# Optimization experiments

Hardware: AMD Instinct MI355X
Metric: run time of the kernel (lower is better)

The kernel has to match this reference:

```python
import jax, jax.numpy as jnp
import numpy as np

B, S, E = 4, 2048, 2048
NH, NKV, HD = 16, 4, 128  # num_heads, num_kv_heads, head_dim
GROUP = NH // NKV


def setup_inputs() -> dict:
    key = jax.random.key(0)
    ks = jax.random.split(key, 6)
    sc = 0.02
    return {
        "hidden_states": jax.random.normal(ks[0], (B, S, E), dtype=jnp.float32),
        "q_w": jax.random.normal(ks[1], (E, NH * HD), dtype=jnp.float32) * sc,
        "k_w": jax.random.normal(ks[2], (E, NKV * HD), dtype=jnp.float32) * sc,
        "v_w": jax.random.normal(ks[3], (E, NKV * HD), dtype=jnp.float32) * sc,
        "out_w": jax.random.normal(ks[4], (NH * HD, E), dtype=jnp.float32) * sc,
        "out_b": jnp.zeros((E,), dtype=jnp.float32),
    }


def reference(hidden_states, q_w, k_w, v_w, out_w, out_b):
    x = hidden_states
    # projections (no bias on q/k/v, bias on out_proj)
    q = (x @ q_w).reshape(B, S, NH, HD).transpose(0, 2, 1, 3)    # [B,NH,S,HD]
    k = (x @ k_w).reshape(B, S, NKV, HD).transpose(0, 2, 1, 3)   # [B,NKV,S,HD]
    v = (x @ v_w).reshape(B, S, NKV, HD).transpose(0, 2, 1, 3)   # [B,NKV,S,HD]

    # GQA: each kv head serves GROUP consecutive query heads (matches loop order)
    k_exp = jnp.repeat(k, GROUP, axis=1)  # [B,NH,S,HD]
    v_exp = jnp.repeat(v, GROUP, axis=1)

    # GPT-Neo: fp32 attention, NO 1/sqrt(d) scaling
    qf = q.astype(jnp.float32)
    kf = k_exp.astype(jnp.float32)
    scores = jnp.einsum("bhqd,bhkd->bhqk", qf, kf)  # [B,NH,S,S]

    causal = jnp.tril(jnp.ones((S, S), dtype=bool))[None, None]
    mask_value = jnp.finfo(scores.dtype).min
    scores = jnp.where(causal, scores, mask_value)

    attn = jax.nn.softmax(scores, axis=-1).astype(v.dtype)
    ctx = jnp.einsum("bhqk,bhkd->bhqd", attn, v_exp)  # [B,NH,S,HD]

    out = ctx.transpose(0, 2, 1, 3).reshape(B, S, NH * HD)
    return out @ out_w + out_b
```

## Files before the change

### kernel.cpp

```cpp
#include <hip/hip_runtime.h>

typedef unsigned short u16;
typedef unsigned int   u32;
typedef __attribute__((ext_vector_type(8))) _Float16 f16x8;
typedef __attribute__((ext_vector_type(2))) __fp16   fp16x2;
typedef __attribute__((ext_vector_type(4))) float    f32x4;

#define LOG2E 1.44269504088896340f

__device__ __forceinline__ u16 f2h(float x) {
  union { _Float16 h; u16 u; } c;
  c.h = (_Float16)x;
  return c.u;
}
__device__ __forceinline__ u32 pk2(float a, float b) {
  union { fp16x2 h; u32 u; } c;
  c.h = __builtin_amdgcn_cvt_pkrtz(a, b);
  return c.u;
}
__device__ __forceinline__ void swap32(u32& a, u32& b) {
  asm volatile("v_permlane32_swap_b32 %0, %1" : "+v"(a), "+v"(b));
}
__device__ __forceinline__ void swap16(u32& a, u32& b) {
  asm volatile("v_permlane16_swap_b32 %0, %1" : "+v"(a), "+v"(b));
}
__device__ __forceinline__ void gload16(const u16* g, u16* l) {
  __builtin_amdgcn_global_load_lds(
      (const __attribute__((address_space(1))) void*)g,
      (__attribute__((address_space(3))) void*)l, 16, 0, 0);
}
__device__ __forceinline__ f32x4 MFMA(f16x8 a, f16x8 b, f32x4 c) {
  return __builtin_amdgcn_mfma_f32_16x16x32_f16(a, b, c, 0, 0, 0);
}

__global__ void conv_f16(const float4* __restrict__ src, u16* __restrict__ d, int n4) {
  int i = blockIdx.x * 256 + threadIdx.x;
  if (i >= n4) return;
  float4 v = src[i];
  union { u16 u[4]; uint2 q; } H;
  H.u[0] = f2h(v.x); H.u[1] = f2h(v.y); H.u[2] = f2h(v.z); H.u[3] = f2h(v.w);
  *(uint2*)&d[(size_t)i * 4] = H.q;
}

__global__ void transpose_f16(const float* __restrict__ src, int K, int N,
                              u16* __restrict__ d, int rowOff) {
  __shared__ float t[32][33];
  int n0 = blockIdx.x * 32, k0 = blockIdx.y * 32;
  int tx = threadIdx.x, ty = threadIdx.y;
#pragma unroll
  for (int i = 0; i < 4; ++i)
    t[ty + 8 * i][tx] = src[(size_t)(k0 + ty + 8 * i) * N + n0 + tx];
  __syncthreads();
#pragma unroll
  for (int i = 0; i < 4; ++i) {
    int n = n0 + ty + 8 * i, k = k0 + tx;
    d[(size_t)(rowOff + n) * 2048 + k] = f2h(t[tx][ty + 8 * i]);
  }
}

__global__ __launch_bounds__(512) void gemm_qkv(
    const u16* __restrict__ A, const u16* __restrict__ B,
    u16* __restrict__ Qf, u16* __restrict__ Kf, u16* __restrict__ VT) {
  const int K = 2048;
  const int NS = K / 32;
  __shared__ u16 As[3][256 * 32];
  __shared__ u16 Bs[3][128 * 32];
  int tid = threadIdx.x;
  int l = tid & 63, w = tid >> 6;
  int lr = l & 15, lg = l >> 4;
  int wr = w >> 1, wc = w & 1;
  int r0 = tid >> 2;
  int ssrc = (((tid & 3) ^ ((r0 >> 1) & 3))) * 8;
  size_t half = (size_t)128 * K;
  int swz = (lr >> 1) & 3;
  int aoff = (wr * 64 + lr) * 32 + (lg ^ swz) * 8;
  int boff = (wc * 64 + lr) * 32 + (lg ^ swz) * 8;

  for (int job = blockIdx.x; job < 768; job += 512) {
    int lidx = (job & 7) * 96 + (job >> 3);
    int bx = lidx % 24, by = lidx / 24;
    int rowA = by * 256, colB = bx * 128;
    const u16* ga = A + (size_t)(rowA + r0) * K + ssrc;
    const u16* gb = B + (size_t)(colB + r0) * K + ssrc;
    f32x4 acc[4][4] = {};

    gload16(ga, &As[0][tid * 8]);
    gload16(ga + half, &As[0][4096 + tid * 8]);
    gload16(gb, &Bs[0][tid * 8]);
    gload16(ga + 32, &As[1][tid * 8]);
    gload16(ga + 32 + half, &As[1][4096 + tid * 8]);
    gload16(gb + 32, &Bs[1][tid * 8]);
    asm volatile("s_waitcnt vmcnt(3)" ::: "memory");
    __builtin_amdgcn_sched_barrier(0);
    __builtin_amdgcn_s_barrier();
    __builtin_amdgcn_sched_barrier(0);

    for (int t = 0; t < NS; ++t) {
      int cur = t % 3, nxt = (t + 2) % 3;
      bool pre = (t + 2 < NS);
      int kb2 = (t + 2) * 32;
      f16x8 ah[4], bh[4];
#pragma unroll
      for (int i = 0; i < 4; ++i)
        ah[i] = *(const f16x8*)&As[cur][aoff + i * 512];
#pragma unroll
      for (int j = 0; j < 4; ++j)
        bh[j] = *(const f16x8*)&Bs[cur][boff + j * 512];
      if (pre) {
        gload16(ga + kb2, &As[nxt][tid * 8]);
        gload16(ga + kb2 + half, &As[nxt][4096 + tid * 8]);
        gload16(gb + kb2, &Bs[nxt][tid * 8]);
      }
      __builtin_amdgcn_s_setprio(1);
#pragma unroll
      for (int i = 0; i < 4; ++i)
#pragma unroll
        for (int j = 0; j < 4; ++j)
          acc[i][j] = MFMA(ah[i], bh[j], acc[i][j]);
      __builtin_amdgcn_s_setprio(0);
      if (pre) {
        asm volatile("s_waitcnt vmcnt(3)" ::: "memory");
      } else {
        asm volatile("s_waitcnt vmcnt(0)" ::: "memory");
      }
      __builtin_amdgcn_sched_barrier(0);
      __builtin_amdgcn_s_barrier();
      __builtin_amdgcn_sched_barrier(0);
    }

#pragma unroll
    for (int i = 0; i < 4; ++i) {
      int row0 = rowA + wr * 64 + i * 16 + lg * 4;
#pragma unroll
      for (int j = 0; j < 4; ++j) {
        int c = colB + wc * 64 + j * 16 + lr;
        f32x4 v = acc[i][j];
        if (c < 2048) {
#pragma unroll
          for (int r = 0; r < 4; ++r)
            Qf[(size_t)(row0 + r) * 2048 + c] = f2h(v[r]);
        } else if (c < 2560) {
          int ck = c - 2048;
#pragma unroll
          for (int r = 0; r < 4; ++r)
            Kf[(size_t)(row0 + r) * 512 + ck] = f2h(v[r]);
        } else {
          int cv = c - 2560, kvh = cv >> 7, d = cv & 127;
          int b = row0 >> 11, t2 = row0 & 2047;
          union { u16 u[4]; uint2 q; } P;
#pragma unroll
          for (int r = 0; r < 4; ++r) P.u[r] = f2h(v[r]);
          *(uint2*)&VT[((size_t)(b * 4 + kvh) * 128 + d) * 2048 + t2] = P.q;
        }
      }
    }
    __builtin_amdgcn_s_barrier();
    __builtin_amdgcn_sched_barrier(0);
  }
}

__global__ __launch_bounds__(512) void gemm_out(
    const u16* __restrict__ A, const u16* __restrict__ B,
    float* __restrict__ Out, const float* __restrict__ bias) {
  const int K = 2048;
  const int NS = K / 64;
  __shared__ u16 As[2][256 * 64];
  __shared__ u16 Bs[2][256 * 64];
  int tid = threadIdx.x;
  int l = tid & 63, w = tid >> 6;
  int lr = l & 15, lg = l >> 4;
  int wm = w >> 2, wn = w & 3;
  int p = blockIdx.x;
  int lidx = (p & 7) * 32 + (p >> 3);
  int bx = lidx & 7, by = lidx >> 3;
  int rowA = by * 256, colB = bx * 256;
  int srow = tid >> 3, sslot = tid & 7;
  int soff = ((sslot ^ (srow & 7))) * 8;
  const u16* ga = A + (size_t)(rowA + srow) * K + soff;
  const u16* gb = B + (size_t)(colB + srow) * K + soff;
  size_t sweep = (size_t)64 * K;
  f32x4 acc[8][4] = {};

  auto STAGE_A = [&](int kb, int bi) {
#pragma unroll
    for (int i = 0; i < 4; ++i)
      gload16(ga + i * sweep + kb, &As[bi][i * 4096 + tid * 8]);
  };
  auto STAGE_B = [&](int kb, int bi) {
#pragma unroll
    for (int i = 0; i < 4; ++i)
      gload16(gb + i * sweep + kb, &Bs[bi][i * 4096 + tid * 8]);
  };

  STAGE_A(0, 0);
  STAGE_B(0, 0);
  asm volatile("s_waitcnt vmcnt(0)" ::: "memory");
  __builtin_amdgcn_sched_barrier(0);
  __builtin_amdgcn_s_barrier();
  __builtin_amdgcn_sched_barrier(0);

  for (int t = 0; t < NS; ++t) {
    int cur = t & 1, nxt = cur ^ 1;
    bool pre = (t + 1 < NS);
    int kb1 = (t + 1) * 64;
    const u16* Ab = &As[cur][0];
    const u16* Bb = &Bs[cur][0];
    f16x8 afr[4][2], bfr[4][2];
#pragma unroll
    for (int mi = 0; mi < 4; ++mi)
#pragma unroll
      for (int kk = 0; kk < 2; ++kk) {
        int row = wm * 128 + mi * 16 + lr;
        afr[mi][kk] = *(const f16x8*)&Ab[row * 64 + (((kk * 4 + lg) ^ (row & 7)) * 8)];
      }
#pragma unroll
    for (int nj = 0; nj < 2; ++nj)
#pragma unroll
      for (int kk = 0; kk < 2; ++kk) {
        int row = wn * 64 + nj * 16 + lr;
        bfr[nj][kk] = *(const f16x8*)&Bb[row * 64 + (((kk * 4 + lg) ^ (row & 7)) * 8)];
      }
    if (pre) STAGE_A(kb1, nxt);
    __builtin_amdgcn_s_setprio(1);
#pragma unroll
    for (int mi = 0; mi < 4; ++mi)
#pragma unroll
      for (int nj = 0; nj < 2; ++nj) {
        acc[mi][nj] = MFMA(afr[mi][0], bfr[nj][0], acc[mi][nj]);
        acc[mi][nj] = MFMA(afr[mi][1], bfr[nj][1], acc[mi][nj]);
      }
    __builtin_amdgcn_s_setprio(0);
    __builtin_amdgcn_s_barrier();
#pragma unroll
    for (int nj = 2; nj < 4; ++nj)
#pragma unroll
      for (int kk = 0; kk < 2; ++kk) {
        int row = wn * 64 + nj * 16 + lr;
        bfr[nj][kk] = *(const f16x8*)&Bb[row * 64 + (((kk * 4 + lg) ^ (row & 7)) * 8)];
      }
    if (pre) STAGE_B(kb1, nxt);
    __builtin_amdgcn_s_setprio(1);
#pragma unroll
    for (int mi = 0; mi < 4; ++mi)
#pragma unroll
      for (int nj = 2; nj < 4; ++nj) {
        acc[mi][nj] = MFMA(afr[mi][0], bfr[nj][0], acc[mi][nj]);
        acc[mi][nj] = MFMA(afr[mi][1], bfr[nj][1], acc[mi][nj]);
      }
    __builtin_amdgcn_s_setprio(0);
    __builtin_amdgcn_s_barrier();
#pragma unroll
    for (int mi = 0; mi < 4; ++mi)
#pragma unroll
      for (int kk = 0; kk < 2; ++kk) {
        int row = wm * 128 + 64 + mi * 16 + lr;
        afr[mi][kk] = *(const f16x8*)&Ab[row * 64 + (((kk * 4 + lg) ^ (row & 7)) * 8)];
      }
    __builtin_amdgcn_s_setprio(1);
#pragma unroll
    for (int mi = 0; mi < 4; ++mi)
#pragma unroll
      for (int nj = 0; nj < 2; ++nj) {
        acc[4 + mi][nj] = MFMA(afr[mi][0], bfr[nj][0], acc[4 + mi][nj]);
        acc[4 + mi][nj] = MFMA(afr[mi][1], bfr[nj][1], acc[4 + mi][nj]);
      }
    __builtin_amdgcn_s_setprio(0);
    __builtin_amdgcn_s_barrier();
    __builtin_amdgcn_s_setprio(1);
#pragma unroll
    for (int mi = 0; mi < 4; ++mi)
#pragma unroll
      for (int nj = 2; nj < 4; ++nj) {
        acc[4 + mi][nj] = MFMA(afr[mi][0], bfr[nj][0], acc[4 + mi][nj]);
        acc[4 + mi][nj] = MFMA(afr[mi][1], bfr[nj][1], acc[4 + mi][nj]);
      }
    __builtin_amdgcn_s_setprio(0);
    asm volatile("s_waitcnt vmcnt(0)" ::: "memory");
    __builtin_amdgcn_sched_barrier(0);
    __builtin_amdgcn_s_barrier();
    __builtin_amdgcn_sched_barrier(0);
  }

#pragma unroll
  for (int mi = 0; mi < 8; ++mi) {
    int row0 = rowA + wm * 128 + mi * 16 + lg * 4;
#pragma unroll
    for (int nj = 0; nj < 4; ++nj) {
      int c = colB + wn * 64 + nj * 16 + lr;
      float bb = bias[c];
#pragma unroll
      for (int r = 0; r < 4; ++r)
        Out[(size_t)(row0 + r) * 2048 + c] = acc[mi][nj][r] + bb;
    }
  }
}

__global__ __launch_bounds__(512) void attn_kernel(
    const u16* __restrict__ Qf, const u16* __restrict__ Kf,
    const u16* __restrict__ VT, u16* __restrict__ Ch) {
  __shared__ u16 Ks[2][64 * 128];
  __shared__ u16 Vs[2][128 * 64];

  int tid = threadIdx.x;
  int w = tid >> 6, l = tid & 63;
  int lr = l & 15, lg = l >> 4;

  int p = blockIdx.x;
  int bid = (p & 7) * 64 + (p >> 3);
  int pair = bid & 7;
  int hg = (bid >> 3) & 3;
  int kvh = (bid >> 5) & 3;
  int b = bid >> 7;
  int h = kvh * 4 + hg;

  const u16* Kb = Kf + (size_t)(b * 2048) * 512 + kvh * 128;
  const u16* Vb = VT + (size_t)((b * 4 + kvh) * 128) * 2048;

  auto STAGE_K = [&](int t, int bufi) {
    int kv0 = t * 64;
#pragma unroll
    for (int pp = 0; pp < 2; ++pp) {
      int o16 = pp * 512 + tid;
      int krow = o16 >> 4;
      int kslot = ((o16 & 15) ^ (krow & 7)) * 8;
      gload16(Kb + (size_t)(kv0 + krow) * 512 + kslot, &Ks[bufi][o16 * 8]);
    }
  };
  auto STAGE_V = [&](int t, int bufi) {
    int kv0 = t * 64;
#pragma unroll
    for (int pp = 0; pp < 2; ++pp) {
      int o16 = pp * 512 + tid;
      int vrow = o16 >> 3;
      int vslot = ((o16 & 7) ^ (vrow & 7)) * 8;
      gload16(Vb + (size_t)vrow * 2048 + kv0 + vslot, &Vs[bufi][o16 * 8]);
    }
  };

  for (int pass = 0; pass < 2; ++pass) {
    int tIdx = pass == 0 ? (15 - pair) : pair;
    int q0 = tIdx * 128;
    int qr0 = q0 + w * 16;
    int nt = q0 / 64 + 2;

    size_t qbase = (size_t)(b * 2048 + qr0 + lr) * 2048 + h * 128 + lg * 8;
    f16x8 qf[4];
#pragma unroll
    for (int d = 0; d < 4; ++d)
      qf[d] = *(const f16x8*)(Qf + qbase + d * 32);

    f32x4 o[8] = {};
    float mrun = -3e38f;
    float lp = 0.f;

    STAGE_K(0, 0);
    STAGE_V(0, 0);
    asm volatile("s_waitcnt vmcnt(0)" ::: "memory");
    __builtin_amdgcn_sched_barrier(0);
    __builtin_amdgcn_s_barrier();
    __builtin_amdgcn_sched_barrier(0);

    int cur = 0;
    for (int t = 0; t < nt; ++t) {
      int kv0 = t * 64;
      bool more = (t + 1 < nt);
      if (more) {
        STAGE_K(t + 1, cur ^ 1);
        STAGE_V(t + 1, cur ^ 1);
      }
      bool compute = (kv0 <= qr0 + 15);

      if (compute) {
        f32x4 s[4] = {};
        __builtin_amdgcn_s_setprio(1);
#pragma unroll
        for (int d = 0; d < 4; ++d) {
#pragma unroll
          for (int n = 0; n < 4; ++n) {
            int row = n * 16 + lr;
            int sl = ((d * 4 + lg) ^ (row & 7)) * 8;
            f16x8 kf = *(const f16x8*)&Ks[cur][row * 128 + sl];
            s[n] = MFMA(kf, qf[d], s[n]);
          }
        }
        __builtin_amdgcn_s_setprio(0);
        if (kv0 + 63 > qr0) {
#pragma unroll
          for (int n = 0; n < 4; ++n)
#pragma unroll
            for (int r = 0; r < 4; ++r)
              if (kv0 + n * 16 + lg * 4 + r > qr0 + lr) s[n][r] = -3e38f;
        }
        float m0 = fmaxf(fmaxf(s[0][0], s[0][1]), fmaxf(s[0][2], s[0][3]));
        float m1 = fmaxf(fmaxf(s[1][0], s[1][1]), fmaxf(s[1][2], s[1][3]));
        float m2 = fmaxf(fmaxf(s[2][0], s[2][1]), fmaxf(s[2][2], s[2][3]));
        float m3 = fmaxf(fmaxf(s[3][0], s[3][1]), fmaxf(s[3][2], s[3][3]));
        float rowmax = fmaxf(fmaxf(m0, m1), fmaxf(m2, m3));
        if (__any(rowmax > mrun + 8.f)) {
          float tm = rowmax;
          tm = fmaxf(tm, __shfl_xor(tm, 16));
          tm = fmaxf(tm, __shfl_xor(tm, 32));
          float mn = fmaxf(mrun, tm);
          float alpha = __builtin_amdgcn_exp2f((mrun - mn) * LOG2E);
          mrun = mn;
          lp *= alpha;
#pragma unroll
          for (int dt = 0; dt < 8; ++dt)
#pragma unroll
            for (int r = 0; r < 4; ++r) o[dt][r] *= alpha;
        }
        float mL = mrun * LOG2E;
        float pv[4][4];
#pragma unroll
        for (int n = 0; n < 4; ++n)
#pragma unroll
          for (int r = 0; r < 4; ++r) {
            pv[n][r] = __builtin_amdgcn_exp2f(fmaf(s[n][r], LOG2E, -mL));
            lp += pv[n][r];
          }
        u32 A0[4], A1[4];
#pragma unroll
        for (int n = 0; n < 4; ++n) {
          A0[n] = pk2(pv[n][0], pv[n][1]);
          A1[n] = pk2(pv[n][2], pv[n][3]);
        }
        swap32(A0[0], A0[2]); swap32(A0[1], A0[3]);
        swap32(A1[0], A1[2]); swap32(A1[1], A1[3]);
        swap16(A0[0], A0[2]); swap16(A0[1], A0[3]);
        swap16(A1[0], A1[2]); swap16(A1[1], A1[3]);
        swap32(A0[0], A0[1]); swap32(A0[2], A0[3]);
        swap32(A1[0], A1[1]); swap32(A1[2], A1[3]);
        union { u32 w4[4]; f16x8 v; } P0, P1;
        P0.w4[0] = A0[0]; P0.w4[1] = A1[0]; P0.w4[2] = A0[2]; P0.w4[3] = A1[2];
        P1.w4[0] = A0[1]; P1.w4[1] = A1[1]; P1.w4[2] = A0[3]; P1.w4[3] = A1[3];
        __builtin_amdgcn_s_setprio(1);
#pragma unroll
        for (int n2 = 0; n2 < 2; ++n2) {
          f16x8 pf = n2 ? P1.v : P0.v;
#pragma unroll
          for (int dt = 0; dt < 8; ++dt) {
            int d = dt * 16 + lr;
            f16x8 vf = *(const f16x8*)&Vs[cur][d * 64 + (((n2 * 4 + lg) ^ (lr & 7)) * 8)];
            o[dt] = MFMA(vf, pf, o[dt]);
          }
        }
        __builtin_amdgcn_s_setprio(0);
      }
      asm volatile("s_waitcnt vmcnt(0) lgkmcnt(0)" ::: "memory");
      __builtin_amdgcn_sched_barrier(0);
      __builtin_amdgcn_s_barrier();
      __builtin_amdgcn_sched_barrier(0);
      cur ^= 1;
    }
    lp += __shfl_xor(lp, 16);
    lp += __shfl_xor(lp, 32);
    float inv = 1.0f / lp;
    size_t orow = (size_t)(b * 2048 + qr0 + lr) * 2048 + h * 128 + lg * 4;
#pragma unroll
    for (int dt = 0; dt < 8; ++dt) {
      uint2 pkt;
      pkt.x = pk2(o[dt][0] * inv, o[dt][1] * inv);
      pkt.y = pk2(o[dt][2] * inv, o[dt][3] * inv);
      *(uint2*)&Ch[orow + dt * 16] = pkt;
    }
  }
}

extern "C" void kernel_launch(void* const* d_in, const int* in_sizes, int n_in,
                              void* d_out, int out_size, void* d_ws, size_t ws_size,
                              hipStream_t stream) {
  const float* X  = (const float*)d_in[0];
  const float* qw = (const float*)d_in[1];
  const float* kw = (const float*)d_in[2];
  const float* vw = (const float*)d_in[3];
  const float* ow = (const float*)d_in[4];
  const float* ob = (const float*)d_in[5];
  float* Out = (float*)d_out;

  char* ws = (char*)d_ws;
  size_t off = 0;
  auto alloc = [&](size_t bytes) -> void* {
    void* p = ws + off;
    off += (bytes + 255) & ~(size_t)255;
    return p;
  };
  const size_t MK = (size_t)8192 * 2048;
  u16* Xf = (u16*)alloc(MK * 2);
  u16* Bt = (u16*)alloc((size_t)3072 * 2048 * 2);
  u16* OW = (u16*)alloc((size_t)2048 * 2048 * 2);
  u16* Qf = (u16*)alloc(MK * 2);
  u16* Kf = (u16*)alloc((size_t)8192 * 512 * 2);
  u16* VT = (u16*)alloc((size_t)8192 * 512 * 2);
  u16* Ch = (u16*)alloc(MK * 2);

  conv_f16<<<dim3(16384), dim3(256), 0, stream>>>((const float4*)X, Xf, (int)(MK / 4));
  dim3 tb(32, 8);
  transpose_f16<<<dim3(64, 64), tb, 0, stream>>>(qw, 2048, 2048, Bt, 0);
  transpose_f16<<<dim3(16, 64), tb, 0, stream>>>(kw, 2048, 512, Bt, 2048);
  transpose_f16<<<dim3(16, 64), tb, 0, stream>>>(vw, 2048, 512, Bt, 2560);
  transpose_f16<<<dim3(64, 64), tb, 0, stream>>>(ow, 2048, 2048, OW, 0);
  gemm_qkv<<<dim3(512), dim3(512), 0, stream>>>(Xf, Bt, Qf, Kf, VT);
  attn_kernel<<<dim3(512), dim3(512), 0, stream>>>(Qf, Kf, VT, Ch);
  gemm_out<<<dim3(256), dim3(512), 0, stream>>>(Ch, OW, Out, ob);
}
```

Baseline: 323.7 us.

## Retile QKV GEMM to 256x256 tiles with double-buffered BK=64 pipeline

The QKV projection GEMM moves from 256x128 tiles with a triple-buffered K=32 pipeline and a persistent 768-job loop to 256x256 tiles with a double-buffered K=64 pipeline, using the same interleaved load/MFMA schedule as the output GEMM. It launches exactly 384 blocks with one tile each, which removes the tail of the 768-jobs-over-512-blocks loop and raises arithmetic intensity per loaded byte. The cost is more accumulator registers (8x4 fragments), a larger LDS footprint and fewer blocks than CUs. The V-transpose store now writes scalars per row instead of a packed uint2.

```diff
diff --git a/kernel.cpp b/kernel.cpp
--- a/kernel.cpp
+++ b/kernel.cpp
@@ -62,100 +62,150 @@
     const u16* __restrict__ A, const u16* __restrict__ B,
     u16* __restrict__ Qf, u16* __restrict__ Kf, u16* __restrict__ VT) {
   const int K = 2048;
-  const int NS = K / 32;
-  __shared__ u16 As[3][256 * 32];
-  __shared__ u16 Bs[3][128 * 32];
+  const int NS = K / 64;
+  __shared__ u16 As[2][256 * 64];
+  __shared__ u16 Bs[2][256 * 64];
   int tid = threadIdx.x;
   int l = tid & 63, w = tid >> 6;
   int lr = l & 15, lg = l >> 4;
-  int wr = w >> 1, wc = w & 1;
-  int r0 = tid >> 2;
-  int ssrc = (((tid & 3) ^ ((r0 >> 1) & 3))) * 8;
-  size_t half = (size_t)128 * K;
-  int swz = (lr >> 1) & 3;
-  int aoff = (wr * 64 + lr) * 32 + (lg ^ swz) * 8;
-  int boff = (wc * 64 + lr) * 32 + (lg ^ swz) * 8;
-
-  for (int job = blockIdx.x; job < 768; job += 512) {
-    int lidx = (job & 7) * 96 + (job >> 3);
-    int bx = lidx % 24, by = lidx / 24;
-    int rowA = by * 256, colB = bx * 128;
-    const u16* ga = A + (size_t)(rowA + r0) * K + ssrc;
-    const u16* gb = B + (size_t)(colB + r0) * K + ssrc;
-    f32x4 acc[4][4] = {};
-
-    gload16(ga, &As[0][tid * 8]);
-    gload16(ga + half, &As[0][4096 + tid * 8]);
-    gload16(gb, &Bs[0][tid * 8]);
-    gload16(ga + 32, &As[1][tid * 8]);
-    gload16(ga + 32 + half, &As[1][4096 + tid * 8]);
-    gload16(gb + 32, &Bs[1][tid * 8]);
-    asm volatile("s_waitcnt vmcnt(3)" ::: "memory");
+  int wm = w >> 2, wn = w & 3;
+  int p = blockIdx.x;
+  int lidx = (p & 7) * 48 + (p >> 3);
+  int bx = lidx % 12, by = lidx / 12;
+  int rowA = by * 256, colB = bx * 256;
+  int srow = tid >> 3, sslot = tid & 7;
+  int soff = ((sslot ^ (srow & 7))) * 8;
+  const u16* ga = A + (size_t)(rowA + srow) * K + soff;
+  const u16* gb = B + (size_t)(colB + srow) * K + soff;
+  size_t sweep = (size_t)64 * K;
+  f32x4 acc[8][4] = {};
+
+  auto STAGE_A = [&](int kb, int bi) {
+#pragma unroll
+    for (int i = 0; i < 4; ++i)
+      gload16(ga + i * sweep + kb, &As[bi][i * 4096 + tid * 8]);
+  };
+  auto STAGE_B = [&](int kb, int bi) {
+#pragma unroll
+    for (int i = 0; i < 4; ++i)
+      gload16(gb + i * sweep + kb, &Bs[bi][i * 4096 + tid * 8]);
+  };
+
+  STAGE_A(0, 0);
+  STAGE_B(0, 0);
+  asm volatile("s_waitcnt vmcnt(0)" ::: "memory");
+  __builtin_amdgcn_sched_barrier(0);
+  __builtin_amdgcn_s_barrier();
+  __builtin_amdgcn_sched_barrier(0);
+
+  for (int t = 0; t < NS; ++t) {
+    int cur = t & 1, nxt = cur ^ 1;
+    bool pre = (t + 1 < NS);
+    int kb1 = (t + 1) * 64;
+    const u16* Ab = &As[cur][0];
+    const u16* Bb = &Bs[cur][0];
+    f16x8 afr[4][2], bfr[4][2];
+#pragma unroll
+    for (int mi = 0; mi < 4; ++mi)
+#pragma unroll
+      for (int kk = 0; kk < 2; ++kk) {
+        int row = wm * 128 + mi * 16 + lr;
+        afr[mi][kk] = *(const f16x8*)&Ab[row * 64 + (((kk * 4 + lg) ^ (row & 7)) * 8)];
+      }
+#pragma unroll
+    for (int nj = 0; nj < 2; ++nj)
+#pragma unroll
+      for (int kk = 0; kk < 2; ++kk) {
+        int row = wn * 64 + nj * 16 + lr;
+        bfr[nj][kk] = *(const f16x8*)&Bb[row * 64 + (((kk * 4 + lg) ^ (row & 7)) * 8)];
+      }
+    if (pre) STAGE_A(kb1, nxt);
+    __builtin_amdgcn_s_setprio(1);
+#pragma unroll
+    for (int mi = 0; mi < 4; ++mi)
+#pragma unroll
+      for (int nj = 0; nj < 2; ++nj) {
+        acc[mi][nj] = MFMA(afr[mi][0], bfr[nj][0], acc[mi][nj]);
+        acc[mi][nj] = MFMA(afr[mi][1], bfr[nj][1], acc[mi][nj]);
+      }
+    __builtin_amdgcn_s_setprio(0);
+    __builtin_amdgcn_s_barrier();
+#pragma unroll
+    for (int nj = 2; nj < 4; ++nj)
+#pragma unroll
+      for (int kk = 0; kk < 2; ++kk) {
+        int row = wn * 64 + nj * 16 + lr;
+        bfr[nj][kk] = *(const f16x8*)&Bb[row * 64 + (((kk * 4 + lg) ^ (row & 7)) * 8)];
+      }
+    if (pre) STAGE_B(kb1, nxt);
+    __builtin_amdgcn_s_setprio(1);
+#pragma unroll
+    for (int mi = 0; mi < 4; ++mi)
+#pragma unroll
+      for (int nj = 2; nj < 4; ++nj) {
+        acc[mi][nj] = MFMA(afr[mi][0], bfr[nj][0], acc[mi][nj]);
+        acc[mi][nj] = MFMA(afr[mi][1], bfr[nj][1], acc[mi][nj]);
+      }
+    __builtin_amdgcn_s_setprio(0);
+    __builtin_amdgcn_s_barrier();
+#pragma unroll
+    for (int mi = 0; mi < 4; ++mi)
+#pragma unroll
+      for (int kk = 0; kk < 2; ++kk) {
+        int row = wm * 128 + 64 + mi * 16 + lr;
+        afr[mi][kk] = *(const f16x8*)&Ab[row * 64 + (((kk * 4 + lg) ^ (row & 7)) * 8)];
+      }
+    __builtin_amdgcn_s_setprio(1);
+#pragma unroll
+    for (int mi = 0; mi < 4; ++mi)
+#pragma unroll
+      for (int nj = 0; nj < 2; ++nj) {
+        acc[4 + mi][nj] = MFMA(afr[mi][0], bfr[nj][0], acc[4 + mi][nj]);
+        acc[4 + mi][nj] = MFMA(afr[mi][1], bfr[nj][1], acc[4 + mi][nj]);
+      }
+    __builtin_amdgcn_s_setprio(0);
+    __builtin_amdgcn_s_barrier();
+    __builtin_amdgcn_s_setprio(1);
+#pragma unroll
+    for (int mi = 0; mi < 4; ++mi)
+#pragma unroll
+      for (int nj = 2; nj < 4; ++nj) {
+        acc[4 + mi][nj] = MFMA(afr[mi][0], bfr[nj][0], acc[4 + mi][nj]);
+        acc[4 + mi][nj] = MFMA(afr[mi][1], bfr[nj][1], acc[4 + mi][nj]);
+      }
+    __builtin_amdgcn_s_setprio(0);
+    asm volatile("s_waitcnt vmcnt(0)" ::: "memory");
     __builtin_amdgcn_sched_barrier(0);
     __builtin_amdgcn_s_barrier();
     __builtin_amdgcn_sched_barrier(0);
-
-    for (int t = 0; t < NS; ++t) {
-      int cur = t % 3, nxt = (t + 2) % 3;
-      bool pre = (t + 2 < NS);
-      int kb2 = (t + 2) * 32;
-      f16x8 ah[4], bh[4];
-#pragma unroll
-      for (int i = 0; i < 4; ++i)
-        ah[i] = *(const f16x8*)&As[cur][aoff + i * 512];
-#pragma unroll
-      for (int j = 0; j < 4; ++j)
-        bh[j] = *(const f16x8*)&Bs[cur][boff + j * 512];
-      if (pre) {
-        gload16(ga + kb2, &As[nxt][tid * 8]);
-        gload16(ga + kb2 + half, &As[nxt][4096 + tid * 8]);
-        gload16(gb + kb2, &Bs[nxt][tid * 8]);
-      }
-      __builtin_amdgcn_s_setprio(1);
-#pragma unroll
-      for (int i = 0; i < 4; ++i)
-#pragma unroll
-        for (int j = 0; j < 4; ++j)
-          acc[i][j] = MFMA(ah[i], bh[j], acc[i][j]);
-      __builtin_amdgcn_s_setprio(0);
-      if (pre) {
-        asm volatile("s_waitcnt vmcnt(3)" ::: "memory");
+  }
+
+#pragma unroll
+  for (int mi = 0; mi < 8; ++mi) {
+    int row0 = rowA + wm * 128 + mi * 16 + lg * 4;
+#pragma unroll
+    for (int nj = 0; nj < 4; ++nj) {
+      int c = colB + wn * 64 + nj * 16 + lr;
+      f32x4 v = acc[mi][nj];
+      if (c < 2048) {
+#pragma unroll
+        for (int r = 0; r < 4; ++r)
+          Qf[(size_t)(row0 + r) * 2048 + c] = f2h(v[r]);
+      } else if (c < 2560) {
+        int ck = c - 2048;
+#pragma unroll
+        for (int r = 0; r < 4; ++r)
+          Kf[(size_t)(row0 + r) * 512 + ck] = f2h(v[r]);
       } else {
-        asm volatile("s_waitcnt vmcnt(0)" ::: "memory");
-      }
-      __builtin_amdgcn_sched_barrier(0);
-      __builtin_amdgcn_s_barrier();
-      __builtin_amdgcn_sched_barrier(0);
+        int cv = c - 2560, kvh = cv >> 7, d = cv & 127;
+#pragma unroll
+        for (int r = 0; r < 4; ++r) {
+          int row = row0 + r;
+          int b = row >> 11, t2 = row & 2047;
+          VT[((size_t)(b * 4 + kvh) * 128 + d) * 2048 + t2] = f2h(v[r]);
+        }
+      }
     }
-
-#pragma unroll
-    for (int i = 0; i < 4; ++i) {
-      int row0 = rowA + wr * 64 + i * 16 + lg * 4;
-#pragma unroll
-      for (int j = 0; j < 4; ++j) {
-        int c = colB + wc * 64 + j * 16 + lr;
-        f32x4 v = acc[i][j];
-        if (c < 2048) {
-#pragma unroll
-          for (int r = 0; r < 4; ++r)
-            Qf[(size_t)(row0 + r) * 2048 + c] = f2h(v[r]);
-        } else if (c < 2560) {
-          int ck = c - 2048;
-#pragma unroll
-          for (int r = 0; r < 4; ++r)
-            Kf[(size_t)(row0 + r) * 512 + ck] = f2h(v[r]);
-        } else {
-          int cv = c - 2560, kvh = cv >> 7, d = cv & 127;
-          int b = row0 >> 11, t2 = row0 & 2047;
-          union { u16 u[4]; uint2 q; } P;
-#pragma unroll
-          for (int r = 0; r < 4; ++r) P.u[r] = f2h(v[r]);
-          *(uint2*)&VT[((size_t)(b * 4 + kvh) * 128 + d) * 2048 + t2] = P.q;
-        }
-      }
-    }
-    __builtin_amdgcn_s_barrier();
-    __builtin_amdgcn_sched_barrier(0);
   }
 }
 
@@ -499,7 +549,7 @@
   transpose_f16<<<dim3(16, 64), tb, 0, stream>>>(kw, 2048, 512, Bt, 2048);
   transpose_f16<<<dim3(16, 64), tb, 0, stream>>>(vw, 2048, 512, Bt, 2560);
   transpose_f16<<<dim3(64, 64), tb, 0, stream>>>(ow, 2048, 2048, OW, 0);
-  gemm_qkv<<<dim3(512), dim3(512), 0, stream>>>(Xf, Bt, Qf, Kf, VT);
+  gemm_qkv<<<dim3(384), dim3(512), 0, stream>>>(Xf, Bt, Qf, Kf, VT);
   attn_kernel<<<dim3(512), dim3(512), 0, stream>>>(Qf, Kf, VT, Ch);
   gemm_out<<<dim3(256), dim3(512), 0, stream>>>(Ch, OW, Out, ob);
 }
```

Result: no change. 322.2 us (-0.5%).
